# Kernel optimization log

Hardware: AMD Instinct MI355X
Metric: run time of the kernel (lower is better)

## Reference

```python
import jax, jax.numpy as jnp
import numpy as np

B, T, C, H = 8, 2048, 768, 64  # batch, block_size, n_embd, head_size

def setup_inputs() -> dict:
    key = jax.random.key(0)
    kx, kk, kq, kv = jax.random.split(key, 4)
    x = jax.random.normal(kx, (B, T, C), dtype=jnp.float32)
    Wk = jax.random.normal(kk, (C, H), dtype=jnp.float32) * (C ** -0.5)
    Wq = jax.random.normal(kq, (C, H), dtype=jnp.float32) * (C ** -0.5)
    Wv = jax.random.normal(kv, (C, H), dtype=jnp.float32) * (C ** -0.5)
    return {"x": x, "Wk": Wk, "Wq": Wq, "Wv": Wv}

def reference(x, Wk, Wq, Wv):
    # single causal self-attention head (dropout in eval mode = identity)
    k = jnp.einsum('btc,ch->bth', x, Wk)  # [B,T,H]
    q = jnp.einsum('btc,ch->bth', x, Wq)
    v = jnp.einsum('btc,ch->bth', x, Wv)
    scale = jnp.asarray(k.shape[-1], x.dtype) ** -0.5
    wei = jnp.einsum('bth,bsh->bts', q, k) * scale  # [B,T,T]
    t = x.shape[1]
    causal = jnp.tril(jnp.ones((t, t), dtype=bool))
    wei = jnp.where(causal[None, :, :], wei, jnp.asarray(-jnp.inf, wei.dtype))
    wei = jax.nn.softmax(wei, axis=-1)
    out = jnp.einsum('bts,bsh->bth', wei, v)  # [B,T,H]
    return out
```

## Files before the change

### kernel.cpp

```cpp
#include <hip/hip_runtime.h>
#include <hip/hip_bf16.h>

typedef __attribute__((ext_vector_type(8))) short short8;
typedef __attribute__((ext_vector_type(4))) float f32x4;

#define B_  8
#define T_  2048
#define C_  768
#define H_  64
#define M_  (B_ * T_)

#define GLDS16(g, l) __builtin_amdgcn_global_load_lds(                        \
    (const __attribute__((address_space(1))) void*)(g),                       \
    (__attribute__((address_space(3))) void*)(l), 16, 0, 0)

static __device__ __forceinline__ unsigned short f2bf(float f) {
    __hip_bfloat16 h = __float2bfloat16(f);
    return *reinterpret_cast<unsigned short*>(&h);
}

static __device__ __forceinline__ short8 make_frag(const unsigned short* p0, const unsigned short* p1) {
    const ushort4 a = *reinterpret_cast<const ushort4*>(p0);
    const ushort4 b = *reinterpret_cast<const ushort4*>(p1);
    short8 r;
    r[0] = (short)a.x; r[1] = (short)a.y; r[2] = (short)a.z; r[3] = (short)a.w;
    r[4] = (short)b.x; r[5] = (short)b.y; r[6] = (short)b.z; r[7] = (short)b.w;
    return r;
}

static __device__ __forceinline__ int swz(int row, int u) {
    return row * 64 + ((((u) >> 3) ^ (row & 7)) << 3) + (u & 7);
}

__global__ __launch_bounds__(256) void prep_w(
    const float* __restrict__ Wq, const float* __restrict__ Wk, const float* __restrict__ Wv,
    unsigned short* __restrict__ Wt) {

    const int t   = threadIdx.x;
    const int mat = blockIdx.x / 48;
    const int kb  = blockIdx.x % 48;
    const int h   = t & 63;
    const int k0  = (kb * 4 + (t >> 6)) * 4;

    const float* Ws = (mat == 0) ? Wq : (mat == 1) ? Wk : Wv;
    ushort4 o;
    o.x = f2bf(Ws[(size_t)(k0 + 0) * H_ + h]);
    o.y = f2bf(Ws[(size_t)(k0 + 1) * H_ + h]);
    o.z = f2bf(Ws[(size_t)(k0 + 2) * H_ + h]);
    o.w = f2bf(Ws[(size_t)(k0 + 3) * H_ + h]);
    *reinterpret_cast<ushort4*>(&Wt[(size_t)(mat * 64 + h) * C_ + k0]) = o;
}

__global__ __launch_bounds__(256) void proj_kernel(
    const float* __restrict__ x, const unsigned short* __restrict__ Wt,
    unsigned short* __restrict__ qkv) {

    __shared__ unsigned short Als[4 * 12 * 512];

    const int tid = threadIdx.x;
    const int w   = tid >> 6;
    const int l   = tid & 63;
    const int lg  = l >> 4;
    const int lc  = l & 15;
    const int row0 = blockIdx.x * 64;

    const int sr   = tid >> 2;
    const int so   = tid & 3;
    const int srt  = sr >> 4;
    const int sr15 = sr & 15;
    const int sbase = (so * 16 + (sr15 ^ so)) * 8;

    f32x4 acc[4][3];
#pragma unroll
    for (int rt = 0; rt < 4; ++rt)
#pragma unroll
        for (int ct = 0; ct < 3; ++ct) acc[rt][ct] = (f32x4)0.f;

    const unsigned short* bbase[3];
#pragma unroll
    for (int ct = 0; ct < 3; ++ct)
        bbase[ct] = Wt + (size_t)(w * 48 + ct * 16 + lc) * C_ + lg * 8;

    for (int phase = 0; phase < 2; ++phase) {
        if (phase) __syncthreads();
#pragma unroll
        for (int g = 0; g < 3; ++g) {
            float4 fa[4][2];
#pragma unroll
            for (int jj = 0; jj < 4; ++jj) {
                const int j = g * 4 + jj;
                const float* xp = x + (size_t)(row0 + sr) * C_ + phase * 384 + j * 32 + so * 8;
                fa[jj][0] = *reinterpret_cast<const float4*>(xp);
                fa[jj][1] = *reinterpret_cast<const float4*>(xp + 4);
            }
#pragma unroll
            for (int jj = 0; jj < 4; ++jj) {
                const int j = g * 4 + jj;
                short8 v;
                v[0] = (short)f2bf(fa[jj][0].x); v[1] = (short)f2bf(fa[jj][0].y);
                v[2] = (short)f2bf(fa[jj][0].z); v[3] = (short)f2bf(fa[jj][0].w);
                v[4] = (short)f2bf(fa[jj][1].x); v[5] = (short)f2bf(fa[jj][1].y);
                v[6] = (short)f2bf(fa[jj][1].z); v[7] = (short)f2bf(fa[jj][1].w);
                *reinterpret_cast<short8*>(&Als[(srt * 12 + j) * 512 + sbase]) = v;
            }
        }
        __syncthreads();

        short8 bcur[3], bnxt[3];
#pragma unroll
        for (int ct = 0; ct < 3; ++ct)
            bcur[ct] = *reinterpret_cast<const short8*>(bbase[ct] + phase * 384);

#pragma unroll
        for (int kk = 0; kk < 12; ++kk) {
            if (kk < 11) {
#pragma unroll
                for (int ct = 0; ct < 3; ++ct)
                    bnxt[ct] = *reinterpret_cast<const short8*>(bbase[ct] + phase * 384 + (kk + 1) * 32);
            }
            short8 af[4];
#pragma unroll
            for (int rt = 0; rt < 4; ++rt)
                af[rt] = *reinterpret_cast<const short8*>(
                    &Als[(rt * 12 + kk) * 512 + (lg * 16 + (lc ^ lg)) * 8]);
#pragma unroll
            for (int rt = 0; rt < 4; ++rt)
#pragma unroll
                for (int ct = 0; ct < 3; ++ct)
                    acc[rt][ct] = __builtin_amdgcn_mfma_f32_16x16x32_bf16(af[rt], bcur[ct], acc[rt][ct], 0, 0, 0);
            if (kk < 11) {
#pragma unroll
                for (int ct = 0; ct < 3; ++ct) bcur[ct] = bnxt[ct];
            }
        }
    }

    unsigned short* Qd   = qkv;
    unsigned short* Kimg = qkv + (size_t)M_ * H_;
    unsigned short* Vimg = qkv + (size_t)2 * M_ * H_;
#pragma unroll
    for (int ct = 0; ct < 3; ++ct) {
        const int col = w * 48 + ct * 16 + lc;
        const int mat = col >> 6;
        const int h   = col & 63;
#pragma unroll
        for (int rt = 0; rt < 4; ++rt)
#pragma unroll
            for (int j = 0; j < 4; ++j) {
                const int grow = row0 + rt * 16 + lg * 4 + j;
                const unsigned short v = f2bf(acc[rt][ct][j]);
                if (mat == 0) {
                    Qd[(size_t)grow * H_ + h] = v;
                } else {
                    const int g  = grow >> 6;
                    const int s6 = grow & 63;
                    if (mat == 1) Kimg[((size_t)g << 12) + swz(s6, h)] = v;
                    else          Vimg[((size_t)g << 12) + swz(h, s6)] = v;
                }
            }
    }
}

#define SEG_FLOATS 4224
#define LOG2E_SCALE 0.18033688011112042f

template<int SEG>
static __device__ __forceinline__ int segs_per_batch() { return SEG == 32 ? 32 : 80; }

template<int SEG>
static __device__ __forceinline__ void decode_seg(int r, int& qt, int& seg) {
    if (SEG == 32) { qt = r; seg = 0; return; }
    if (r < 8)       { qt = r;                seg = 0; }
    else if (r < 24) { qt = 8  + (r - 8) / 2; seg = (r - 8) & 1; }
    else if (r < 48) { qt = 16 + (r - 24) / 3; seg = (r - 24) % 3; }
    else             { qt = 24 + (r - 48) / 4; seg = (r - 48) & 3; }
}

template<int SEG>
static __device__ __forceinline__ int seg_prefix(int qt) {
    if (SEG == 32) return qt;
    if (qt < 8)  return qt;
    if (qt < 16) return 8  + 2 * (qt - 8);
    if (qt < 24) return 24 + 3 * (qt - 16);
    return 48 + 4 * (qt - 24);
}

template<int SEG>
__global__ __launch_bounds__(256) void attn_partial(
    const unsigned short* __restrict__ qkv, float* __restrict__ part) {

    const int spb = segs_per_batch<SEG>();
    const int b   = blockIdx.x / spb;
    const int r_  = blockIdx.x % spb;
    int qt, seg;
    decode_seg<SEG>(r_, qt, seg);

    const int tid = threadIdx.x;
    const int w  = tid >> 6;
    const int l  = tid & 63;
    const int lg = l >> 4;
    const int lc = l & 15;

    __shared__ unsigned short Kls[2][4096];
    __shared__ unsigned short Vls[2][4096];

    const unsigned short* Qg = qkv;
    const unsigned short* Kg = qkv + (size_t)M_ * H_;
    const unsigned short* Vg = qkv + (size_t)2 * M_ * H_;

    const unsigned short* qrow = Qg + (size_t)(b * T_ + qt * 64 + w * 16 + lc) * H_;
    short8 qf[2];
#pragma unroll
    for (int ks = 0; ks < 2; ++ks)
        qf[ks] = make_frag(qrow + ks * 32 + lg * 4, qrow + ks * 32 + lg * 4 + 16);

    float mval = -1e30f, lsum = 0.f;
    f32x4 oT[4];
#pragma unroll
    for (int t = 0; t < 4; ++t) oT[t] = (f32x4)0.f;

    const int q_glob = qt * 64 + w * 16 + lc;

    const int kv_beg = seg * SEG;
    const int kv_end = min(kv_beg + SEG, qt + 1);

    const int go = w * 1024 + l * 8;

    auto stage = [&](int buf, int kv) {
        const size_t tb = ((size_t)(b * 32 + kv)) << 12;
        const unsigned short* kt = Kg + tb;
        const unsigned short* vt = Vg + tb;
        GLDS16(kt + go,       &Kls[buf][w * 1024]);
        GLDS16(kt + go + 512, &Kls[buf][w * 1024 + 512]);
        GLDS16(vt + go,       &Vls[buf][w * 1024]);
        GLDS16(vt + go + 512, &Vls[buf][w * 1024 + 512]);
    };

    stage(0, kv_beg);
    int cur = 0;

    for (int kv = kv_beg; kv < kv_end; ++kv) {
        const bool more = (kv + 1 < kv_end);
        __builtin_amdgcn_s_barrier();
        asm volatile("" ::: "memory");
        if (more) {
            stage(cur ^ 1, kv + 1);
            asm volatile("s_waitcnt vmcnt(4)" ::: "memory");
        } else {
            asm volatile("s_waitcnt vmcnt(0)" ::: "memory");
        }
        __builtin_amdgcn_s_barrier();
        asm volatile("" ::: "memory");

        const unsigned short* Kc = Kls[cur];
        const unsigned short* Vc = Vls[cur];

        f32x4 sT[4];
#pragma unroll
        for (int st = 0; st < 4; ++st) {
            f32x4 accs = (f32x4)0.f;
#pragma unroll
            for (int ks = 0; ks < 2; ++ks) {
                const short8 kf = make_frag(&Kc[swz(st * 16 + lc, ks * 32 + lg * 4)],
                                            &Kc[swz(st * 16 + lc, ks * 32 + lg * 4 + 16)]);
                accs = __builtin_amdgcn_mfma_f32_16x16x32_bf16(kf, qf[ks], accs, 0, 0, 0);
            }
            sT[st] = accs;
        }

        float p[4][4];
#pragma unroll
        for (int st = 0; st < 4; ++st)
#pragma unroll
            for (int r = 0; r < 4; ++r)
                p[st][r] = sT[st][r] * LOG2E_SCALE;

        if (kv == qt) {
#pragma unroll
            for (int st = 0; st < 4; ++st)
#pragma unroll
                for (int r = 0; r < 4; ++r)
                    if ((kv * 64 + st * 16 + lg * 4 + r) > q_glob) p[st][r] = -1e30f;
        }

        float pm[4];
#pragma unroll
        for (int st = 0; st < 4; ++st)
            pm[st] = fmaxf(fmaxf(p[st][0], p[st][1]), fmaxf(p[st][2], p[st][3]));
        float pmax = fmaxf(fmaxf(pm[0], pm[1]), fmaxf(pm[2], pm[3]));
        pmax = fmaxf(pmax, __shfl_xor(pmax, 16));
        pmax = fmaxf(pmax, __shfl_xor(pmax, 32));

        if (!__all(pmax <= mval)) {
            const float mnew  = fmaxf(mval, pmax);
            const float alpha = exp2f(mval - mnew);
            mval = mnew;
            lsum *= alpha;
#pragma unroll
            for (int ht = 0; ht < 4; ++ht) oT[ht] *= alpha;
        }

        float ps[4];
#pragma unroll
        for (int st = 0; st < 4; ++st) {
#pragma unroll
            for (int r = 0; r < 4; ++r)
                p[st][r] = exp2f(p[st][r] - mval);
            ps[st] = (p[st][0] + p[st][1]) + (p[st][2] + p[st][3]);
        }
        float srow = (ps[0] + ps[1]) + (ps[2] + ps[3]);
        srow += __shfl_xor(srow, 16);
        srow += __shfl_xor(srow, 32);
        lsum += srow;

        short8 pb[2];
#pragma unroll
        for (int ks = 0; ks < 2; ++ks) {
#pragma unroll
            for (int r = 0; r < 4; ++r) {
                pb[ks][r]     = (short)f2bf(p[2 * ks][r]);
                pb[ks][r + 4] = (short)f2bf(p[2 * ks + 1][r]);
            }
        }

#pragma unroll
        for (int ks = 0; ks < 2; ++ks) {
#pragma unroll
            for (int ht = 0; ht < 4; ++ht) {
                const short8 vf = make_frag(&Vc[swz(ht * 16 + lc, ks * 32 + lg * 4)],
                                            &Vc[swz(ht * 16 + lc, ks * 32 + lg * 4 + 16)]);
                oT[ht] = __builtin_amdgcn_mfma_f32_16x16x32_bf16(vf, pb[ks], oT[ht], 0, 0, 0);
            }
        }
        cur ^= 1;
    }

    float* base = part + (size_t)blockIdx.x * SEG_FLOATS;
#pragma unroll
    for (int ht = 0; ht < 4; ++ht)
        *reinterpret_cast<f32x4*>(&base[(w * 16 + lc) * 64 + ht * 16 + lg * 4]) = oT[ht];
    if (lg == 0) {
        base[4096 + w * 16 + lc] = mval;
        base[4160 + w * 16 + lc] = lsum;
    }
}

template<int SEG>
__global__ __launch_bounds__(256) void attn_merge(
    const float* __restrict__ part, float* __restrict__ out) {

    const int b  = blockIdx.x >> 5;
    const int qt = blockIdx.x & 31;
    const int nseg = (SEG == 32) ? 1 : (qt / 8 + 1);
    const int spb  = segs_per_batch<SEG>();
    const float* base0 = part + (size_t)(b * spb + seg_prefix<SEG>(qt)) * SEG_FLOATS;

    const int tid = threadIdx.x;
    const int row = tid >> 2;
    const int c0  = (tid & 3) * 16;

    float M = -1e30f;
    for (int s = 0; s < nseg; ++s)
        M = fmaxf(M, base0[(size_t)s * SEG_FLOATS + 4096 + row]);

    float L = 0.f;
    f32x4 acc[4];
#pragma unroll
    for (int k = 0; k < 4; ++k) acc[k] = (f32x4)0.f;

    for (int s = 0; s < nseg; ++s) {
        const float* sb = base0 + (size_t)s * SEG_FLOATS;
        const float wsc = exp2f(sb[4096 + row] - M);
        L += sb[4160 + row] * wsc;
#pragma unroll
        for (int k = 0; k < 4; ++k) {
            const f32x4 ov = *reinterpret_cast<const f32x4*>(&sb[row * 64 + c0 + 4 * k]);
            acc[k] += ov * wsc;
        }
    }
    const float inv = 1.f / L;
    float* op = out + (size_t)(b * T_ + qt * 64 + row) * H_ + c0;
#pragma unroll
    for (int k = 0; k < 4; ++k)
        *reinterpret_cast<f32x4*>(&op[4 * k]) = acc[k] * inv;
}

__global__ __launch_bounds__(256) void attn_kernel(
    const unsigned short* __restrict__ qkv, float* __restrict__ out) {

    const int b  = blockIdx.x >> 5;
    const int qt = blockIdx.x & 31;
    const int tid = threadIdx.x;
    const int w  = tid >> 6;
    const int l  = tid & 63;
    const int lg = l >> 4;
    const int lc = l & 15;

    __shared__ unsigned short Kl[4096];
    __shared__ unsigned short Vt[4096];

    const unsigned short* Qg = qkv;
    const unsigned short* Kg = qkv + (size_t)M_ * H_;
    const unsigned short* Vg = qkv + (size_t)2 * M_ * H_;

    const unsigned short* qrow = Qg + (size_t)(b * T_ + qt * 64 + w * 16 + lc) * H_;
    short8 qf[2];
#pragma unroll
    for (int ks = 0; ks < 2; ++ks)
        qf[ks] = make_frag(qrow + ks * 32 + lg * 4, qrow + ks * 32 + lg * 4 + 16);

    float mval = -1e30f, lsum = 0.f;
    f32x4 oT[4];
#pragma unroll
    for (int t = 0; t < 4; ++t) oT[t] = (f32x4)0.f;

    const int q_glob = qt * 64 + w * 16 + lc;

    for (int kv = 0; kv <= qt; ++kv) {
        __syncthreads();
        const size_t tb = ((size_t)(b * 32 + kv)) << 12;
        reinterpret_cast<short8*>(Kl)[tid]       = reinterpret_cast<const short8*>(Kg + tb)[tid];
        reinterpret_cast<short8*>(Kl)[tid + 256] = reinterpret_cast<const short8*>(Kg + tb)[tid + 256];
        reinterpret_cast<short8*>(Vt)[tid]       = reinterpret_cast<const short8*>(Vg + tb)[tid];
        reinterpret_cast<short8*>(Vt)[tid + 256] = reinterpret_cast<const short8*>(Vg + tb)[tid + 256];
        __syncthreads();

        f32x4 sT[4];
#pragma unroll
        for (int st = 0; st < 4; ++st) {
            f32x4 accs = (f32x4)0.f;
#pragma unroll
            for (int ks = 0; ks < 2; ++ks) {
                const short8 kf = make_frag(&Kl[swz(st * 16 + lc, ks * 32 + lg * 4)],
                                            &Kl[swz(st * 16 + lc, ks * 32 + lg * 4 + 16)]);
                accs = __builtin_amdgcn_mfma_f32_16x16x32_bf16(kf, qf[ks], accs, 0, 0, 0);
            }
            sT[st] = accs;
        }

        float p[4][4];
#pragma unroll
        for (int st = 0; st < 4; ++st)
#pragma unroll
            for (int r = 0; r < 4; ++r)
                p[st][r] = sT[st][r] * LOG2E_SCALE;

        if (kv == qt) {
#pragma unroll
            for (int st = 0; st < 4; ++st)
#pragma unroll
                for (int r = 0; r < 4; ++r)
                    if ((kv * 64 + st * 16 + lg * 4 + r) > q_glob) p[st][r] = -1e30f;
        }

        float pm[4];
#pragma unroll
        for (int st = 0; st < 4; ++st)
            pm[st] = fmaxf(fmaxf(p[st][0], p[st][1]), fmaxf(p[st][2], p[st][3]));
        float pmax = fmaxf(fmaxf(pm[0], pm[1]), fmaxf(pm[2], pm[3]));
        pmax = fmaxf(pmax, __shfl_xor(pmax, 16));
        pmax = fmaxf(pmax, __shfl_xor(pmax, 32));

        if (!__all(pmax <= mval)) {
            const float mnew  = fmaxf(mval, pmax);
            const float alpha = exp2f(mval - mnew);
            mval = mnew;
            lsum *= alpha;
#pragma unroll
            for (int ht = 0; ht < 4; ++ht) oT[ht] *= alpha;
        }

        float ps[4];
#pragma unroll
        for (int st = 0; st < 4; ++st) {
#pragma unroll
            for (int r = 0; r < 4; ++r)
                p[st][r] = exp2f(p[st][r] - mval);
            ps[st] = (p[st][0] + p[st][1]) + (p[st][2] + p[st][3]);
        }
        float srow = (ps[0] + ps[1]) + (ps[2] + ps[3]);
        srow += __shfl_xor(srow, 16);
        srow += __shfl_xor(srow, 32);
        lsum += srow;

        short8 pb[2];
#pragma unroll
        for (int ks = 0; ks < 2; ++ks) {
#pragma unroll
            for (int r = 0; r < 4; ++r) {
                pb[ks][r]     = (short)f2bf(p[2 * ks][r]);
                pb[ks][r + 4] = (short)f2bf(p[2 * ks + 1][r]);
            }
        }

#pragma unroll
        for (int ks = 0; ks < 2; ++ks) {
#pragma unroll
            for (int ht = 0; ht < 4; ++ht) {
                const short8 vf = make_frag(&Vt[swz(ht * 16 + lc, ks * 32 + lg * 4)],
                                            &Vt[swz(ht * 16 + lc, ks * 32 + lg * 4 + 16)]);
                oT[ht] = __builtin_amdgcn_mfma_f32_16x16x32_bf16(vf, pb[ks], oT[ht], 0, 0, 0);
            }
        }
    }

    const float inv = 1.f / lsum;
    float* op = out + (size_t)(b * T_ + q_glob) * H_;
#pragma unroll
    for (int ht = 0; ht < 4; ++ht) {
        f32x4 v = oT[ht] * inv;
        *reinterpret_cast<f32x4*>(&op[ht * 16 + lg * 4]) = v;
    }
}

extern "C" void kernel_launch(void* const* d_in, const int* in_sizes, int n_in,
                              void* d_out, int out_size, void* d_ws, size_t ws_size,
                              hipStream_t stream) {
    const float* x  = (const float*)d_in[0];
    const float* Wk = (const float*)d_in[1];
    const float* Wq = (const float*)d_in[2];
    const float* Wv = (const float*)d_in[3];

    const size_t qkvB = (size_t)3 * M_ * H_ * 2;
    const size_t WtB  = (size_t)3 * H_ * C_ * 2;
    unsigned short* qkv = (unsigned short*)d_ws;
    unsigned short* Wt  = (unsigned short*)((char*)d_ws + qkvB);
    float* part = (float*)((char*)d_ws + qkvB + WtB);
    float* out  = (float*)d_out;

    prep_w<<<dim3(144), dim3(256), 0, stream>>>(Wq, Wk, Wv, Wt);
    proj_kernel<<<dim3(M_ / 64), dim3(256), 0, stream>>>(x, Wt, qkv);

    const size_t need8  = qkvB + WtB + (size_t)(B_ * 80) * SEG_FLOATS * 4;
    const size_t need32 = qkvB + WtB + (size_t)(B_ * 32) * SEG_FLOATS * 4;
    if (ws_size >= need8) {
        attn_partial<8><<<dim3(B_ * 80), dim3(256), 0, stream>>>(qkv, part);
        attn_merge<8><<<dim3(B_ * 32), dim3(256), 0, stream>>>(part, out);
    } else if (ws_size >= need32) {
        attn_partial<32><<<dim3(B_ * 32), dim3(256), 0, stream>>>(qkv, part);
        attn_merge<32><<<dim3(B_ * 32), dim3(256), 0, stream>>>(part, out);
    } else {
        attn_kernel<<<dim3(B_ * 32), dim3(256), 0, stream>>>(qkv, out);
    }
}
```

Baseline: 58.38 us.

## Pre-permute K/V tiles for single-load fragments, fold scale into Wq, reverse schedule

The projection kernel now writes K and V tiles in an MFMA-fragment-permuted order, so the attention kernel reads each fragment with one 16-byte LDS load instead of two 8-byte loads. The softmax scale times log2e is folded into the bf16 Wq conversion, which removes a multiply per score. Attention blocks are launched in reverse order so the longest query tiles start first. Single-segment tiles write normalized output directly, and the merge kernel now covers only multi-segment tiles. The extra rounding of the scaled Wq to bf16 changes numerics slightly.

```diff
diff --git a/kernel.cpp b/kernel.cpp
--- a/kernel.cpp
+++ b/kernel.cpp
@@ -32,6 +32,16 @@
     return row * 64 + ((((u) >> 3) ^ (row & 7)) << 3) + (u & 7);
 }
 
+static __device__ __forceinline__ int fragoff(int k) {
+    const int half = k >> 5;
+    const int kk   = k & 31;
+    const int c    = half * 4 + ((kk >> 2) & 3);
+    const int p    = (kk & 3) + ((kk & 16) >> 2);
+    return c * 8 + p;
+}
+
+#define LOG2E_SCALE 0.18033688011112042f
+
 __global__ __launch_bounds__(256) void prep_w(
     const float* __restrict__ Wq, const float* __restrict__ Wk, const float* __restrict__ Wv,
     unsigned short* __restrict__ Wt) {
@@ -43,11 +53,12 @@
     const int k0  = (kb * 4 + (t >> 6)) * 4;
 
     const float* Ws = (mat == 0) ? Wq : (mat == 1) ? Wk : Wv;
+    const float sc  = (mat == 0) ? LOG2E_SCALE : 1.f;
     ushort4 o;
-    o.x = f2bf(Ws[(size_t)(k0 + 0) * H_ + h]);
-    o.y = f2bf(Ws[(size_t)(k0 + 1) * H_ + h]);
-    o.z = f2bf(Ws[(size_t)(k0 + 2) * H_ + h]);
-    o.w = f2bf(Ws[(size_t)(k0 + 3) * H_ + h]);
+    o.x = f2bf(Ws[(size_t)(k0 + 0) * H_ + h] * sc);
+    o.y = f2bf(Ws[(size_t)(k0 + 1) * H_ + h] * sc);
+    o.z = f2bf(Ws[(size_t)(k0 + 2) * H_ + h] * sc);
+    o.w = f2bf(Ws[(size_t)(k0 + 3) * H_ + h] * sc);
     *reinterpret_cast<ushort4*>(&Wt[(size_t)(mat * 64 + h) * C_ + k0]) = o;
 }
 
@@ -138,31 +149,27 @@
     unsigned short* Qd   = qkv;
     unsigned short* Kimg = qkv + (size_t)M_ * H_;
     unsigned short* Vimg = qkv + (size_t)2 * M_ * H_;
+    const size_t g12 = (size_t)blockIdx.x << 12;
 #pragma unroll
     for (int ct = 0; ct < 3; ++ct) {
         const int col = w * 48 + ct * 16 + lc;
         const int mat = col >> 6;
         const int h   = col & 63;
+        const int foh = fragoff(h);
 #pragma unroll
         for (int rt = 0; rt < 4; ++rt)
 #pragma unroll
             for (int j = 0; j < 4; ++j) {
-                const int grow = row0 + rt * 16 + lg * 4 + j;
+                const int s6 = rt * 16 + lg * 4 + j;
                 const unsigned short v = f2bf(acc[rt][ct][j]);
-                if (mat == 0) {
-                    Qd[(size_t)grow * H_ + h] = v;
-                } else {
-                    const int g  = grow >> 6;
-                    const int s6 = grow & 63;
-                    if (mat == 1) Kimg[((size_t)g << 12) + swz(s6, h)] = v;
-                    else          Vimg[((size_t)g << 12) + swz(h, s6)] = v;
-                }
+                if (mat == 0)      Qd[(size_t)(row0 + s6) * H_ + h] = v;
+                else if (mat == 1) Kimg[g12 + swz(s6, foh)] = v;
+                else               Vimg[g12 + swz(h, fragoff(s6))] = v;
             }
     }
 }
 
 #define SEG_FLOATS 4224
-#define LOG2E_SCALE 0.18033688011112042f
 
 template<int SEG>
 static __device__ __forceinline__ int segs_per_batch() { return SEG == 32 ? 32 : 80; }
@@ -187,13 +194,14 @@
 
 template<int SEG>
 __global__ __launch_bounds__(256) void attn_partial(
-    const unsigned short* __restrict__ qkv, float* __restrict__ part) {
+    const unsigned short* __restrict__ qkv, float* __restrict__ part,
+    float* __restrict__ out) {
 
     const int spb = segs_per_batch<SEG>();
     const int b   = blockIdx.x / spb;
-    const int r_  = blockIdx.x % spb;
+    const int rr  = spb - 1 - (blockIdx.x % spb);
     int qt, seg;
-    decode_seg<SEG>(r_, qt, seg);
+    decode_seg<SEG>(rr, qt, seg);
 
     const int tid = threadIdx.x;
     const int w  = tid >> 6;
@@ -261,8 +269,8 @@
             f32x4 accs = (f32x4)0.f;
 #pragma unroll
             for (int ks = 0; ks < 2; ++ks) {
-                const short8 kf = make_frag(&Kc[swz(st * 16 + lc, ks * 32 + lg * 4)],
-                                            &Kc[swz(st * 16 + lc, ks * 32 + lg * 4 + 16)]);
+                const short8 kf = *reinterpret_cast<const short8*>(
+                    &Kc[swz(st * 16 + lc, (ks * 4 + lg) * 8)]);
                 accs = __builtin_amdgcn_mfma_f32_16x16x32_bf16(kf, qf[ks], accs, 0, 0, 0);
             }
             sT[st] = accs;
@@ -273,7 +281,7 @@
         for (int st = 0; st < 4; ++st)
 #pragma unroll
             for (int r = 0; r < 4; ++r)
-                p[st][r] = sT[st][r] * LOG2E_SCALE;
+                p[st][r] = sT[st][r];
 
         if (kv == qt) {
 #pragma unroll
@@ -327,33 +335,42 @@
         for (int ks = 0; ks < 2; ++ks) {
 #pragma unroll
             for (int ht = 0; ht < 4; ++ht) {
-                const short8 vf = make_frag(&Vc[swz(ht * 16 + lc, ks * 32 + lg * 4)],
-                                            &Vc[swz(ht * 16 + lc, ks * 32 + lg * 4 + 16)]);
+                const short8 vf = *reinterpret_cast<const short8*>(
+                    &Vc[swz(ht * 16 + lc, (ks * 4 + lg) * 8)]);
                 oT[ht] = __builtin_amdgcn_mfma_f32_16x16x32_bf16(vf, pb[ks], oT[ht], 0, 0, 0);
             }
         }
         cur ^= 1;
     }
 
-    float* base = part + (size_t)blockIdx.x * SEG_FLOATS;
-#pragma unroll
-    for (int ht = 0; ht < 4; ++ht)
-        *reinterpret_cast<f32x4*>(&base[(w * 16 + lc) * 64 + ht * 16 + lg * 4]) = oT[ht];
-    if (lg == 0) {
-        base[4096 + w * 16 + lc] = mval;
-        base[4160 + w * 16 + lc] = lsum;
-    }
-}
-
-template<int SEG>
-__global__ __launch_bounds__(256) void attn_merge(
+    const int nseg = (SEG == 32) ? 1 : (qt / 8 + 1);
+    if (nseg == 1) {
+        const float inv = 1.f / lsum;
+        float* op = out + (size_t)(b * T_ + q_glob) * H_;
+#pragma unroll
+        for (int ht = 0; ht < 4; ++ht) {
+            f32x4 v = oT[ht] * inv;
+            *reinterpret_cast<f32x4*>(&op[ht * 16 + lg * 4]) = v;
+        }
+    } else {
+        float* base = part + (size_t)(b * spb + seg_prefix<SEG>(qt) + seg) * SEG_FLOATS;
+#pragma unroll
+        for (int ht = 0; ht < 4; ++ht)
+            *reinterpret_cast<f32x4*>(&base[(w * 16 + lc) * 64 + ht * 16 + lg * 4]) = oT[ht];
+        if (lg == 0) {
+            base[4096 + w * 16 + lc] = mval;
+            base[4160 + w * 16 + lc] = lsum;
+        }
+    }
+}
+
+__global__ __launch_bounds__(256) void attn_merge8(
     const float* __restrict__ part, float* __restrict__ out) {
 
-    const int b  = blockIdx.x >> 5;
-    const int qt = blockIdx.x & 31;
-    const int nseg = (SEG == 32) ? 1 : (qt / 8 + 1);
-    const int spb  = segs_per_batch<SEG>();
-    const float* base0 = part + (size_t)(b * spb + seg_prefix<SEG>(qt)) * SEG_FLOATS;
+    const int b  = blockIdx.x / 24;
+    const int qt = 8 + blockIdx.x % 24;
+    const int nseg = qt / 8 + 1;
+    const float* base0 = part + (size_t)(b * 80 + seg_prefix<8>(qt)) * SEG_FLOATS;
 
     const int tid = threadIdx.x;
     const int row = tid >> 2;
@@ -383,134 +400,6 @@
 #pragma unroll
     for (int k = 0; k < 4; ++k)
         *reinterpret_cast<f32x4*>(&op[4 * k]) = acc[k] * inv;
-}
-
-__global__ __launch_bounds__(256) void attn_kernel(
-    const unsigned short* __restrict__ qkv, float* __restrict__ out) {
-
-    const int b  = blockIdx.x >> 5;
-    const int qt = blockIdx.x & 31;
-    const int tid = threadIdx.x;
-    const int w  = tid >> 6;
-    const int l  = tid & 63;
-    const int lg = l >> 4;
-    const int lc = l & 15;
-
-    __shared__ unsigned short Kl[4096];
-    __shared__ unsigned short Vt[4096];
-
-    const unsigned short* Qg = qkv;
-    const unsigned short* Kg = qkv + (size_t)M_ * H_;
-    const unsigned short* Vg = qkv + (size_t)2 * M_ * H_;
-
-    const unsigned short* qrow = Qg + (size_t)(b * T_ + qt * 64 + w * 16 + lc) * H_;
-    short8 qf[2];
-#pragma unroll
-    for (int ks = 0; ks < 2; ++ks)
-        qf[ks] = make_frag(qrow + ks * 32 + lg * 4, qrow + ks * 32 + lg * 4 + 16);
-
-    float mval = -1e30f, lsum = 0.f;
-    f32x4 oT[4];
-#pragma unroll
-    for (int t = 0; t < 4; ++t) oT[t] = (f32x4)0.f;
-
-    const int q_glob = qt * 64 + w * 16 + lc;
-
-    for (int kv = 0; kv <= qt; ++kv) {
-        __syncthreads();
-        const size_t tb = ((size_t)(b * 32 + kv)) << 12;
-        reinterpret_cast<short8*>(Kl)[tid]       = reinterpret_cast<const short8*>(Kg + tb)[tid];
-        reinterpret_cast<short8*>(Kl)[tid + 256] = reinterpret_cast<const short8*>(Kg + tb)[tid + 256];
-        reinterpret_cast<short8*>(Vt)[tid]       = reinterpret_cast<const short8*>(Vg + tb)[tid];
-        reinterpret_cast<short8*>(Vt)[tid + 256] = reinterpret_cast<const short8*>(Vg + tb)[tid + 256];
-        __syncthreads();
-
-        f32x4 sT[4];
-#pragma unroll
-        for (int st = 0; st < 4; ++st) {
-            f32x4 accs = (f32x4)0.f;
-#pragma unroll
-            for (int ks = 0; ks < 2; ++ks) {
-                const short8 kf = make_frag(&Kl[swz(st * 16 + lc, ks * 32 + lg * 4)],
-                                            &Kl[swz(st * 16 + lc, ks * 32 + lg * 4 + 16)]);
-                accs = __builtin_amdgcn_mfma_f32_16x16x32_bf16(kf, qf[ks], accs, 0, 0, 0);
-            }
-            sT[st] = accs;
-        }
-
-        float p[4][4];
-#pragma unroll
-        for (int st = 0; st < 4; ++st)
-#pragma unroll
-            for (int r = 0; r < 4; ++r)
-                p[st][r] = sT[st][r] * LOG2E_SCALE;
-
-        if (kv == qt) {
-#pragma unroll
-            for (int st = 0; st < 4; ++st)
-#pragma unroll
-                for (int r = 0; r < 4; ++r)
-                    if ((kv * 64 + st * 16 + lg * 4 + r) > q_glob) p[st][r] = -1e30f;
-        }
-
-        float pm[4];
-#pragma unroll
-        for (int st = 0; st < 4; ++st)
-            pm[st] = fmaxf(fmaxf(p[st][0], p[st][1]), fmaxf(p[st][2], p[st][3]));
-        float pmax = fmaxf(fmaxf(pm[0], pm[1]), fmaxf(pm[2], pm[3]));
-        pmax = fmaxf(pmax, __shfl_xor(pmax, 16));
-        pmax = fmaxf(pmax, __shfl_xor(pmax, 32));
-
-        if (!__all(pmax <= mval)) {
-            const float mnew  = fmaxf(mval, pmax);
-            const float alpha = exp2f(mval - mnew);
-            mval = mnew;
-            lsum *= alpha;
-#pragma unroll
-            for (int ht = 0; ht < 4; ++ht) oT[ht] *= alpha;
-        }
-
-        float ps[4];
-#pragma unroll
-        for (int st = 0; st < 4; ++st) {
-#pragma unroll
-            for (int r = 0; r < 4; ++r)
-                p[st][r] = exp2f(p[st][r] - mval);
-            ps[st] = (p[st][0] + p[st][1]) + (p[st][2] + p[st][3]);
-        }
-        float srow = (ps[0] + ps[1]) + (ps[2] + ps[3]);
-        srow += __shfl_xor(srow, 16);
-        srow += __shfl_xor(srow, 32);
-        lsum += srow;
-
-        short8 pb[2];
-#pragma unroll
-        for (int ks = 0; ks < 2; ++ks) {
-#pragma unroll
-            for (int r = 0; r < 4; ++r) {
-                pb[ks][r]     = (short)f2bf(p[2 * ks][r]);
-                pb[ks][r + 4] = (short)f2bf(p[2 * ks + 1][r]);
-            }
-        }
-
-#pragma unroll
-        for (int ks = 0; ks < 2; ++ks) {
-#pragma unroll
-            for (int ht = 0; ht < 4; ++ht) {
-                const short8 vf = make_frag(&Vt[swz(ht * 16 + lc, ks * 32 + lg * 4)],
-                                            &Vt[swz(ht * 16 + lc, ks * 32 + lg * 4 + 16)]);
-                oT[ht] = __builtin_amdgcn_mfma_f32_16x16x32_bf16(vf, pb[ks], oT[ht], 0, 0, 0);
-            }
-        }
-    }
-
-    const float inv = 1.f / lsum;
-    float* op = out + (size_t)(b * T_ + q_glob) * H_;
-#pragma unroll
-    for (int ht = 0; ht < 4; ++ht) {
-        f32x4 v = oT[ht] * inv;
-        *reinterpret_cast<f32x4*>(&op[ht * 16 + lg * 4]) = v;
-    }
 }
 
 extern "C" void kernel_launch(void* const* d_in, const int* in_sizes, int n_in,
@@ -531,15 +420,11 @@
     prep_w<<<dim3(144), dim3(256), 0, stream>>>(Wq, Wk, Wv, Wt);
     proj_kernel<<<dim3(M_ / 64), dim3(256), 0, stream>>>(x, Wt, qkv);
 
-    const size_t need8  = qkvB + WtB + (size_t)(B_ * 80) * SEG_FLOATS * 4;
-    const size_t need32 = qkvB + WtB + (size_t)(B_ * 32) * SEG_FLOATS * 4;
+    const size_t need8 = qkvB + WtB + (size_t)(B_ * 80) * SEG_FLOATS * 4;
     if (ws_size >= need8) {
-        attn_partial<8><<<dim3(B_ * 80), dim3(256), 0, stream>>>(qkv, part);
-        attn_merge<8><<<dim3(B_ * 32), dim3(256), 0, stream>>>(part, out);
-    } else if (ws_size >= need32) {
-        attn_partial<32><<<dim3(B_ * 32), dim3(256), 0, stream>>>(qkv, part);
-        attn_merge<32><<<dim3(B_ * 32), dim3(256), 0, stream>>>(part, out);
+        attn_partial<8><<<dim3(B_ * 80), dim3(256), 0, stream>>>(qkv, part, out);
+        attn_merge8<<<dim3(B_ * 24), dim3(256), 0, stream>>>(part, out);
     } else {
-        attn_kernel<<<dim3(B_ * 32), dim3(256), 0, stream>>>(qkv, out);
-    }
-}
+        attn_partial<32><<<dim3(B_ * 32), dim3(256), 0, stream>>>(qkv, part, out);
+    }
+}
```

Result: faster. 55.77 us (-4.5%).
